# Kernel optimization log

Measured on AMD Instinct MI355X. Metric: run time of the kernel, lower is better.

The kernel has to match this reference:

```python
import jax, jax.numpy as jnp
import numpy as np

MARGIN = 1.0
BIG = 1e9  # stand-in for +inf to keep gradients NaN-free

def _l2_normalize(x, eps=1e-12):
    n = jnp.linalg.norm(x, axis=1, keepdims=True)
    return x / jnp.maximum(n, eps)

def setup_inputs() -> dict:
    key = jax.random.key(0)
    k1, k2, k3 = jax.random.split(key, 3)
    B, D = 4096, 1024
    return {
        "text_embeddings": jax.random.normal(k1, (B, D), dtype=jnp.float32),
        "graph_embeddings": jax.random.normal(k2, (B, D), dtype=jnp.float32),
        "labels": jax.random.randint(k3, (B,), 0, 512, dtype=jnp.int64),
    }

def reference(text_embeddings, graph_embeddings, labels):
    B = text_embeddings.shape[0]
    t = _l2_normalize(text_embeddings)
    g = _l2_normalize(graph_embeddings)
    # cosine distance matrix [B, B]
    distances = 1.0 - jnp.matmul(t, g.T)
    pos = jnp.diagonal(distances)                      # [B]
    neg_mask = labels[:, None] != labels[None, :]      # [B, B]
    has_neg = neg_mask.any(axis=1)                     # rows with >=1 negative
    # hard negative mining: per-row min over different-label columns
    hard_neg = jnp.min(jnp.where(neg_mask, distances, BIG), axis=1)
    per_row = jnp.where(has_neg, jax.nn.relu(pos - hard_neg + MARGIN), 0.0)
    triplet_loss = jnp.sum(per_row) / B
    return triplet_loss, distances
```

## Files before the change

kernel.cpp:

```cpp
#include <hip/hip_runtime.h>
#include <hip/hip_bf16.h>


typedef int i32x4 __attribute__((ext_vector_type(4)));

__device__ __forceinline__ void gload16(const void* g, void* l) {
  __builtin_amdgcn_global_load_lds(
      (__attribute__((address_space(1))) void*)(g),
      (__attribute__((address_space(3))) void*)(l), 16, 0, 0);
}

__device__ __forceinline__ int fkey(float x) {
  int u = __float_as_int(x);
  return u >= 0 ? u : (u ^ 0x7fffffff);
}
__device__ __forceinline__ float funkey(int k) {
  return __int_as_float(k >= 0 ? k : (k ^ 0x7fffffff));
}

__global__ __launch_bounds__(256) void k_quant(
    const float* __restrict__ t, const float* __restrict__ g,
    char4* __restrict__ qt, char4* __restrict__ qg,
    float* __restrict__ st, float* __restrict__ sg,
    int* __restrict__ hn_key, int D) {
  const int row = blockIdx.x;
  const float* src = (blockIdx.y ? g : t) + (size_t)row * D;
  char4*      dst  = (blockIdx.y ? qg : qt) + (size_t)row * (D >> 2);
  float*      sout = blockIdx.y ? sg : st;

  float4 v = ((const float4*)src)[threadIdx.x];
  float ss = v.x * v.x + v.y * v.y + v.z * v.z + v.w * v.w;
  float am = fmaxf(fmaxf(fabsf(v.x), fabsf(v.y)), fmaxf(fabsf(v.z), fabsf(v.w)));
#pragma unroll
  for (int off = 32; off; off >>= 1) {
    ss += __shfl_down(ss, off);
    am = fmaxf(am, __shfl_down(am, off));
  }
  __shared__ float rs[4], rm[4];
  if ((threadIdx.x & 63) == 0) { rs[threadIdx.x >> 6] = ss; rm[threadIdx.x >> 6] = am; }
  __syncthreads();
  const float ssT = rs[0] + rs[1] + rs[2] + rs[3];
  const float amT = fmaxf(fmaxf(rm[0], rm[1]), fmaxf(rm[2], rm[3]));
  const float qs  = 127.0f / fmaxf(amT, 1e-20f);

  char4 o;
  o.x = (char)__float2int_rn(v.x * qs);
  o.y = (char)__float2int_rn(v.y * qs);
  o.z = (char)__float2int_rn(v.z * qs);
  o.w = (char)__float2int_rn(v.w * qs);
  dst[threadIdx.x] = o;

  if (threadIdx.x == 0) {
    sout[row] = fmaxf(amT, 1e-20f) / (127.0f * fmaxf(sqrtf(ssT), 1e-12f));
    if (blockIdx.y == 0) hn_key[row] = __float_as_int(1e9f);
  }
}

__global__ __launch_bounds__(256, 2) void k_gemm_fused(
    const char* __restrict__ A, const char* __restrict__ Bm,
    const float* __restrict__ sA, const float* __restrict__ sB,
    const int* __restrict__ labels, float* __restrict__ Dout,
    int* __restrict__ hn_key, float* __restrict__ pos, int N, int K) {
  __shared__ __align__(16) char Atile[2][128 * 128];
  __shared__ __align__(16) char Btile[2][128 * 128];
  __shared__ int   labR[128], labC[128], hnmin[128];
  __shared__ float sAr[128], sBc[128];

  const int tid  = threadIdx.x;
  const int lane = tid & 63;
  const int w    = tid >> 6;
  const int waveM = w >> 1, waveN = w & 1;

  const int nb  = N >> 7;
  const int bid = blockIdx.x;
  int brow, bcol;
  if (nb == 32) {
    const int xcd = bid & 7;
    const int idx = bid >> 3;
    brow = ((xcd >> 2) << 4) + (idx >> 3);
    bcol = ((xcd & 3) << 3) + (idx & 7);
  } else {
    const int cpx = (nb * nb) >> 3;
    const int swz = (bid & 7) * cpx + (bid >> 3);
    brow = swz / nb; bcol = swz % nb;
  }
  const int rowBase = brow * 128;
  const int colBase = bcol * 128;

  const int rr   = tid >> 3;
  const int scol = ((tid & 7) ^ (rr & 7)) << 4;
  const char* aS = A  + (size_t)(rowBase + rr) * K + scol;
  const char* bS = Bm + (size_t)(colBase + rr) * K + scol;
  const int ldsDst = tid * 16;

  const int sw  = (lane & 7) << 4;
  const int khi = (lane >> 4) << 4;
  const int kx0 = khi ^ sw;
  const int kx1 = (64 + khi) ^ sw;
  const int aOffBase = (waveM * 64 + (lane & 15)) * 128;
  const int bOffBase = (waveN * 64 + (lane & 15)) * 128;

#pragma unroll
  for (int q = 0; q < 4; ++q) {
    gload16(aS + (size_t)q * 32 * K, &Atile[0][q * 4096 + ldsDst]);
    gload16(bS + (size_t)q * 32 * K, &Btile[0][q * 4096 + ldsDst]);
  }
  if (tid < 128) {
    labR[tid]  = labels[rowBase + tid];
    sAr[tid]   = sA[rowBase + tid];
    hnmin[tid] = __float_as_int(1e9f);
  } else {
    labC[tid - 128] = labels[colBase + (tid - 128)];
    sBc[tid - 128]  = sB[colBase + (tid - 128)];
  }
  __syncthreads();

  i32x4 acc[4][4];
#pragma unroll
  for (int m = 0; m < 4; ++m)
#pragma unroll
    for (int n = 0; n < 4; ++n) acc[m][n] = (i32x4){0, 0, 0, 0};

  const int NT = K >> 7;
  for (int t = 0; t < NT; ++t) {
    const int cur = t & 1;
    const char* Ab = &Atile[cur][0];
    const char* Bb = &Btile[cur][0];
    const bool pre = (t + 1 < NT);

    if (pre) {
      const size_t koff = (size_t)(t + 1) * 128;
      char* An = &Atile[cur ^ 1][0];
      char* Bn = &Btile[cur ^ 1][0];
#pragma unroll
      for (int q = 0; q < 4; ++q) {
        gload16(aS + (size_t)q * 32 * K + koff, An + q * 4096 + ldsDst);
        gload16(bS + (size_t)q * 32 * K + koff, Bn + q * 4096 + ldsDst);
      }
    }

    i32x4 af[4][2], bf[4][2];
#pragma unroll
    for (int mq = 0; mq < 4; ++mq) {
      const int ro = aOffBase + mq * 2048;
      af[mq][0] = *(const i32x4*)(Ab + ro + kx0);
      af[mq][1] = *(const i32x4*)(Ab + ro + kx1);
    }
#pragma unroll
    for (int nq = 0; nq < 4; ++nq) {
      const int ro = bOffBase + nq * 2048;
      bf[nq][0] = *(const i32x4*)(Bb + ro + kx0);
      bf[nq][1] = *(const i32x4*)(Bb + ro + kx1);
    }

    __builtin_amdgcn_s_setprio(1);
#pragma unroll
    for (int ks = 0; ks < 2; ++ks)
#pragma unroll
      for (int mq = 0; mq < 4; ++mq)
#pragma unroll
        for (int nq = 0; nq < 4; ++nq)
          acc[mq][nq] = __builtin_amdgcn_mfma_i32_16x16x64_i8(
              af[mq][ks], bf[nq][ks], acc[mq][nq], 0, 0, 0);
    __builtin_amdgcn_s_setprio(0);

    if (pre) {
      asm volatile("s_waitcnt vmcnt(0)" ::: "memory");
      __builtin_amdgcn_s_barrier();
      asm volatile("" ::: "memory");
    }
  }

  const int ci = lane & 15;
  const int r4 = (lane >> 4) << 2;
  const bool diagBlk = (rowBase == colBase);
#pragma unroll
  for (int m = 0; m < 4; ++m) {
    const int gilB = waveM * 64 + m * 16 + r4;
#pragma unroll
    for (int r = 0; r < 4; ++r) {
      const int gil = gilB + r;
      const int li  = labR[gil];
      const float sa = sAr[gil];
      const size_t gi = (size_t)(rowBase + gil);
      float mn = 1e9f;
#pragma unroll
      for (int n = 0; n < 4; ++n) {
        const int gjl = waveN * 64 + n * 16 + ci;
        const float d = 1.0f - sa * sBc[gjl] * (float)acc[m][n][r];
        Dout[gi * N + (colBase + gjl)] = d;
        if (labC[gjl] != li) mn = fminf(mn, d);
        if (diagBlk && gil == gjl) pos[gi] = d;
      }
#pragma unroll
      for (int off = 1; off < 16; off <<= 1) mn = fminf(mn, __shfl_xor(mn, off));
      if (ci == 0) atomicMin(&hnmin[gil], fkey(mn));
    }
  }
  __syncthreads();
  if (tid < 128) atomicMin(&hn_key[rowBase + tid], hnmin[tid]);
}

__global__ __launch_bounds__(256) void k_final(
    const int* __restrict__ hn_key, const float* __restrict__ pos,
    float* __restrict__ out, int N) {
  float s = 0.f;
  for (int i = threadIdx.x; i < N; i += 256) {
    const float hn = funkey(hn_key[i]);
    const float pr = pos[i] - hn + 1.0f;
    s += pr > 0.f ? pr : 0.f;
  }
#pragma unroll
  for (int off = 32; off; off >>= 1) s += __shfl_down(s, off);
  __shared__ float red[4];
  if ((threadIdx.x & 63) == 0) red[threadIdx.x >> 6] = s;
  __syncthreads();
  if (threadIdx.x == 0) out[0] = (red[0] + red[1] + red[2] + red[3]) / (float)N;
}

extern "C" void kernel_launch(void* const* d_in, const int* in_sizes, int n_in,
                              void* d_out, int out_size, void* d_ws, size_t ws_size,
                              hipStream_t stream) {
  const float* t      = (const float*)d_in[0];
  const float* g      = (const float*)d_in[1];
  const int*   labels = (const int*)d_in[2];
  const int Bn = in_sizes[2];
  const int D  = in_sizes[0] / Bn;

  float* out  = (float*)d_out;
  float* dist = out + 1;

  char*  qT     = (char*)d_ws;
  char*  qG     = qT + (size_t)Bn * D;
  float* sT     = (float*)(qG + (size_t)Bn * D);
  float* sG     = sT + Bn;
  int*   hn_key = (int*)(sG + Bn);
  float* pos    = (float*)(hn_key + Bn);

  k_quant<<<dim3(Bn, 2), 256, 0, stream>>>(t, g, (char4*)qT, (char4*)qG,
                                           sT, sG, hn_key, D);
  const int nb = Bn / 128;
  k_gemm_fused<<<dim3(nb * nb), 256, 0, stream>>>(qT, qG, sT, sG, labels, dist,
                                                  hn_key, pos, Bn, D);
  k_final<<<1, 256, 0, stream>>>(hn_key, pos, out, Bn);
}
```

Baseline: 52.73 us.

## Drop LDS double buffering in fused GEMM to fit four blocks per CU

```diff
diff --git a/kernel.cpp b/kernel.cpp
--- a/kernel.cpp
+++ b/kernel.cpp
@@ -56,13 +56,13 @@
   }
 }
 
-__global__ __launch_bounds__(256, 2) void k_gemm_fused(
+__global__ __launch_bounds__(256, 4) void k_gemm_fused(
     const char* __restrict__ A, const char* __restrict__ Bm,
     const float* __restrict__ sA, const float* __restrict__ sB,
     const int* __restrict__ labels, float* __restrict__ Dout,
     int* __restrict__ hn_key, float* __restrict__ pos, int N, int K) {
-  __shared__ __align__(16) char Atile[2][128 * 128];
-  __shared__ __align__(16) char Btile[2][128 * 128];
+  __shared__ __align__(16) char Atile[128 * 128];
+  __shared__ __align__(16) char Btile[128 * 128];
   __shared__ int   labR[128], labC[128], hnmin[128];
   __shared__ float sAr[128], sBc[128];
 
@@ -100,11 +100,6 @@
   const int aOffBase = (waveM * 64 + (lane & 15)) * 128;
   const int bOffBase = (waveN * 64 + (lane & 15)) * 128;
 
-#pragma unroll
-  for (int q = 0; q < 4; ++q) {
-    gload16(aS + (size_t)q * 32 * K, &Atile[0][q * 4096 + ldsDst]);
-    gload16(bS + (size_t)q * 32 * K, &Btile[0][q * 4096 + ldsDst]);
-  }
   if (tid < 128) {
     labR[tid]  = labels[rowBase + tid];
     sAr[tid]   = sA[rowBase + tid];
@@ -113,7 +108,6 @@
     labC[tid - 128] = labels[colBase + (tid - 128)];
     sBc[tid - 128]  = sB[colBase + (tid - 128)];
   }
-  __syncthreads();
 
   i32x4 acc[4][4];
 #pragma unroll
@@ -123,34 +117,26 @@
 
   const int NT = K >> 7;
   for (int t = 0; t < NT; ++t) {
-    const int cur = t & 1;
-    const char* Ab = &Atile[cur][0];
-    const char* Bb = &Btile[cur][0];
-    const bool pre = (t + 1 < NT);
-
-    if (pre) {
-      const size_t koff = (size_t)(t + 1) * 128;
-      char* An = &Atile[cur ^ 1][0];
-      char* Bn = &Btile[cur ^ 1][0];
-#pragma unroll
-      for (int q = 0; q < 4; ++q) {
-        gload16(aS + (size_t)q * 32 * K + koff, An + q * 4096 + ldsDst);
-        gload16(bS + (size_t)q * 32 * K + koff, Bn + q * 4096 + ldsDst);
-      }
-    }
+    const size_t koff = (size_t)t * 128;
+#pragma unroll
+    for (int q = 0; q < 4; ++q) {
+      gload16(aS + (size_t)q * 32 * K + koff, &Atile[q * 4096 + ldsDst]);
+      gload16(bS + (size_t)q * 32 * K + koff, &Btile[q * 4096 + ldsDst]);
+    }
+    __syncthreads();
 
     i32x4 af[4][2], bf[4][2];
 #pragma unroll
     for (int mq = 0; mq < 4; ++mq) {
       const int ro = aOffBase + mq * 2048;
-      af[mq][0] = *(const i32x4*)(Ab + ro + kx0);
-      af[mq][1] = *(const i32x4*)(Ab + ro + kx1);
+      af[mq][0] = *(const i32x4*)(Atile + ro + kx0);
+      af[mq][1] = *(const i32x4*)(Atile + ro + kx1);
     }
 #pragma unroll
     for (int nq = 0; nq < 4; ++nq) {
       const int ro = bOffBase + nq * 2048;
-      bf[nq][0] = *(const i32x4*)(Bb + ro + kx0);
-      bf[nq][1] = *(const i32x4*)(Bb + ro + kx1);
+      bf[nq][0] = *(const i32x4*)(Btile + ro + kx0);
+      bf[nq][1] = *(const i32x4*)(Btile + ro + kx1);
     }
 
     __builtin_amdgcn_s_setprio(1);
@@ -164,11 +150,7 @@
               af[mq][ks], bf[nq][ks], acc[mq][nq], 0, 0, 0);
     __builtin_amdgcn_s_setprio(0);
 
-    if (pre) {
-      asm volatile("s_waitcnt vmcnt(0)" ::: "memory");
-      __builtin_amdgcn_s_barrier();
-      asm volatile("" ::: "memory");
-    }
+    __syncthreads();
   }
 
   const int ci = lane & 15;
```

After: 81.03 us. 1.54x slower.
